# Performance work log

Measured on AMD Instinct MI355X. Metric: run time of the kernel, lower is better.

Reference implementation:

```python
import jax, jax.numpy as jnp
import numpy as np

TI, N, TO, D, H, FF, V, L = 128, 8, 32, 512, 8, 2048, 2000, 6


def _ln(x, s, b, eps=1e-5):
    m = jnp.mean(x, -1, keepdims=True)
    v = jnp.var(x, -1, keepdims=True)
    return (x - m) / jnp.sqrt(v + eps) * s + b


def _pos_enc(t, d):
    pos = np.arange(t)[:, None]
    div = np.exp(np.arange(0, d, 2) * (-np.log(10000.0) / d))
    pe = np.zeros((t, d), np.float32)
    pe[:, 0::2] = np.sin(pos * div)
    pe[:, 1::2] = np.cos(pos * div)
    return jnp.asarray(pe)


def _forward(enc_out, embed, enc_w, enc_b, qkv_w, qkv_b, o_w, o_b, ln1_s, ln1_b,
             ff1_w, ff1_b, ff2_w, ff2_b, ln2_s, ln2_b, out_w, tgt_pad, tgt_len, sos):
    n, to = tgt_pad.shape
    t = to + 1
    v, d = embed.shape
    hd = d // H
    # prepend <sos>, embed (scaled) + sinusoidal positions; dropout omitted (eval)
    tgt = jnp.pad(tgt_pad, ((0, 0), (1, 0)), constant_values=sos)  # N x T
    x = embed[tgt] * jnp.sqrt(jnp.float32(d)) + _pos_enc(t, d)[None]  # N x T x D
    x = x.transpose(1, 0, 2)  # T x N x D (time-major, pytorch default)
    causal = jnp.triu(jnp.ones((t, t), bool), k=1)  # True = masked
    lens = jnp.maximum(tgt_len, 1)
    pad = jnp.arange(t)[None, :] >= lens[:, None]  # N x T key padding
    mask = causal[None, None] | pad[:, None, None, :]
    neg = jnp.float32(-1e9)

    def heads(z):  # T x N x D -> N x H x T x hd
        return z.reshape(t, n, H, hd).transpose(1, 2, 0, 3)

    for l in range(L):  # post-norm TransformerEncoderLayer, relu FFN
        qkv = jnp.einsum('tnd,ed->tne', x, qkv_w[l]) + qkv_b[l]
        q, k_, v_ = jnp.split(qkv, 3, axis=-1)
        q = heads(q) / jnp.sqrt(jnp.float32(hd))
        k_, v_ = heads(k_), heads(v_)
        sc = jnp.einsum('nhqd,nhkd->nhqk', q, k_)
        att = jax.nn.softmax(jnp.where(mask, neg, sc), axis=-1)
        o = jnp.einsum('nhqk,nhkd->nhqd', att, v_).transpose(2, 0, 1, 3).reshape(t, n, d)
        o = jnp.einsum('tnd,ed->tne', o, o_w[l]) + o_b[l]
        x = _ln(x + o, ln1_s[l], ln1_b[l])
        h = jax.nn.relu(jnp.einsum('tnd,fd->tnf', x, ff1_w[l]) + ff1_b[l])
        h = jnp.einsum('tnf,df->tnd', h, ff2_w[l]) + ff2_b[l]
        x = _ln(x + h, ln2_s[l], ln2_b[l])

    enc = jnp.einsum('ind,ed->ine', enc_out, enc_w) + enc_b  # Ti x N x D
    add = jnp.tanh(enc[None] + x[:, None])  # (To+1) x Ti x N x D joiner
    out = jnp.einsum('tind,vd->tinv', add, out_w)  # (To+1) x Ti x N x V
    return out.transpose(2, 1, 0, 3)  # N x Ti x (To+1) x V


def setup_inputs() -> dict:
    key = jax.random.key(0)
    ks = jax.random.split(key, 12)
    s = 0.02
    return dict(
        enc_out=jax.random.normal(ks[0], (TI, N, D), jnp.float32),
        embed=jax.random.normal(ks[1], (V, D), jnp.float32) * s,
        enc_w=jax.random.normal(ks[2], (D, D), jnp.float32) * s,
        enc_b=jnp.zeros((D,), jnp.float32),
        qkv_w=jax.random.normal(ks[3], (L, 3 * D, D), jnp.float32) * s,
        qkv_b=jnp.zeros((L, 3 * D), jnp.float32),
        o_w=jax.random.normal(ks[4], (L, D, D), jnp.float32) * s,
        o_b=jnp.zeros((L, D), jnp.float32),
        ln1_s=jnp.ones((L, D), jnp.float32),
        ln1_b=jnp.zeros((L, D), jnp.float32),
        ff1_w=jax.random.normal(ks[5], (L, FF, D), jnp.float32) * s,
        ff1_b=jnp.zeros((L, FF), jnp.float32),
        ff2_w=jax.random.normal(ks[6], (L, D, FF), jnp.float32) * s,
        ff2_b=jnp.zeros((L, D), jnp.float32),
        ln2_s=jnp.ones((L, D), jnp.float32),
        ln2_b=jnp.zeros((L, D), jnp.float32),
        out_w=jax.random.normal(ks[7], (V, D), jnp.float32) * s,
        tgt_pad=jax.random.randint(ks[8], (N, TO), 0, V),
        tgt_len=jax.random.randint(ks[9], (N,), TO // 2, TO + 2),
        sos=1,
    )


def reference(enc_out, embed, enc_w, enc_b, qkv_w, qkv_b, o_w, o_b, ln1_s, ln1_b,
              ff1_w, ff1_b, ff2_w, ff2_b, ln2_s, ln2_b, out_w, tgt_pad, tgt_len, sos):
    return _forward(enc_out, embed, enc_w, enc_b, qkv_w, qkv_b, o_w, o_b, ln1_s, ln1_b,
                    ff1_w, ff1_b, ff2_w, ff2_b, ln2_s, ln2_b, out_w, tgt_pad, tgt_len, sos)
```

## Files before the change

### kernel.cpp

```cpp
#include <hip/hip_runtime.h>
#include <hip/hip_bf16.h>
#include <math.h>

#define TI 128
#define NB 8
#define TO 32
#define TT 33
#define D 512
#define NH 8
#define HD 64
#define FF 2048
#define V 2000
#define NL 6
#define NTOK (TT*NB)
#define MJ (NB*TI*TT)

typedef __attribute__((ext_vector_type(4))) float  f4;
typedef __attribute__((ext_vector_type(8))) short  shortx8;
typedef unsigned short u16;

__device__ __forceinline__ u16 f2bf(float f) {
    unsigned u = __float_as_uint(f);
    unsigned r = (u + 0x7fffu + ((u >> 16) & 1u)) >> 16;
    return (u16)r;
}
__device__ __forceinline__ float bf2f(u16 h) {
    return __uint_as_float(((unsigned)h) << 16);
}
__device__ __forceinline__ float wsum(float v) {
#pragma unroll
    for (int off = 32; off; off >>= 1) v += __shfl_xor(v, off, 64);
    return v;
}
__device__ __forceinline__ float wmax(float v) {
#pragma unroll
    for (int off = 32; off; off >>= 1) v = fmaxf(v, __shfl_xor(v, off, 64));
    return v;
}
__device__ __forceinline__ f4 mfma16(shortx8 a, shortx8 b, f4 c) {
    return __builtin_amdgcn_mfma_f32_16x16x32_bf16(a, b, c, 0, 0, 0);
}
__device__ __forceinline__ void async16(const void* g, void* l) {
    __builtin_amdgcn_global_load_lds(
        (const __attribute__((address_space(1))) unsigned int*)g,
        (__attribute__((address_space(3))) unsigned int*)l, 16, 0, 0);
}

__global__ __launch_bounds__(256) void convert_w(
    const float* __restrict__ q, const float* __restrict__ o,
    const float* __restrict__ f1, const float* __restrict__ f2,
    const float* __restrict__ e, u16* __restrict__ Wh, u16* __restrict__ Wl)
{
    int i4 = blockIdx.x * 256 + threadIdx.x;
    const float* src; int loc;
    if (i4 < 1179648)      { src = q;  loc = i4; }
    else if (i4 < 1572864) { src = o;  loc = i4 - 1179648; }
    else if (i4 < 3145728) { src = f1; loc = i4 - 1572864; }
    else if (i4 < 4718592) { src = f2; loc = i4 - 3145728; }
    else                   { src = e;  loc = i4 - 4718592; }
    f4 v = *(const f4*)(src + (size_t)loc * 4);
    ushort4 h, l;
    h.x = f2bf(v[0]); l.x = f2bf(v[0] - bf2f(h.x));
    h.y = f2bf(v[1]); l.y = f2bf(v[1] - bf2f(h.y));
    h.z = f2bf(v[2]); l.z = f2bf(v[2] - bf2f(h.z));
    h.w = f2bf(v[3]); l.w = f2bf(v[3] - bf2f(h.w));
    *(ushort4*)(Wh + (size_t)i4 * 4) = h;
    *(ushort4*)(Wl + (size_t)i4 * 4) = l;
}

__global__ __launch_bounds__(256) void convert_plane(
    const float* __restrict__ src, u16* __restrict__ dh, u16* __restrict__ dl, int n4)
{
    int i = blockIdx.x * 256 + threadIdx.x;
    if (i >= n4) return;
    f4 v = *(const f4*)(src + (size_t)i * 4);
    ushort4 h, l;
    h.x = f2bf(v[0]); l.x = f2bf(v[0] - bf2f(h.x));
    h.y = f2bf(v[1]); l.y = f2bf(v[1] - bf2f(h.y));
    h.z = f2bf(v[2]); l.z = f2bf(v[2] - bf2f(h.z));
    h.w = f2bf(v[3]); l.w = f2bf(v[3] - bf2f(h.w));
    *(ushort4*)(dh + (size_t)i * 4) = h;
    *(ushort4*)(dl + (size_t)i * 4) = l;
}

__global__ __launch_bounds__(256) void embed_kernel(
    const float* __restrict__ emb, const int* __restrict__ tgt_pad,
    const int* __restrict__ sos, float* __restrict__ x,
    u16* __restrict__ xh, u16* __restrict__ xl)
{
    int idx = blockIdx.x * 256 + threadIdx.x;
    if (idx >= NTOK * D) return;
    int d = idx & (D - 1);
    int row = idx >> 9;
    int t = row >> 3, n = row & 7;
    int tok = (t == 0) ? *sos : tgt_pad[n * TO + t - 1];
    float freq = __expf((float)(d & ~1) * (-0.017988946039015984f));
    float ang = (float)t * freq;
    float pe = (d & 1) ? cosf(ang) : sinf(ang);
    float v = emb[tok * D + d] * 22.627416997969522f + pe;
    x[idx] = v;
    u16 h = f2bf(v);
    xh[idx] = h;
    xl[idx] = f2bf(v - bf2f(h));
}

template<int MODE>
__global__ __launch_bounds__(256) void gemm_bf(
    const u16* __restrict__ Ah, const u16* __restrict__ Al, int lda,
    const u16* __restrict__ Bh, const u16* __restrict__ Bl, int ldb,
    const float* __restrict__ bias,
    float* __restrict__ C, u16* __restrict__ Ch, u16* __restrict__ Cl,
    int M, int N, int ldc, int ksteps)
{
    __shared__ u16 ls[4][64 * 64];
    const int tid = threadIdx.x, lane = tid & 63, w = tid >> 6;
    const int wr = (w >> 1) * 32, wc = (w & 1) * 32;
    const int m0 = blockIdx.x * 64, n0 = blockIdx.y * 64;
    const int qd = lane >> 4, mm = lane & 15;
    const int kb = (MODE == 1) ? (int)blockIdx.z * ksteps * 64 : 0;
    f4 acc[2][2] = {};
    const u16* Ab  = Ah + (size_t)m0 * lda + kb;
    const u16* Alb = Al + (size_t)m0 * lda + kb;
    const u16* Bb  = Bh + (size_t)n0 * ldb + kb;
    const u16* Blb = Bl + (size_t)n0 * ldb + kb;

    for (int it = 0; it < ksteps; ++it) {
        int k0 = it * 64;
        __syncthreads();
#pragma unroll
        for (int i = 0; i < 2; ++i) {
            int idx = tid + i * 256;
            int row = idx >> 3, c8 = (idx & 7) * 8;
            async16(Ab  + (size_t)row * lda + k0 + c8, &ls[0][idx * 8]);
            async16(Alb + (size_t)row * lda + k0 + c8, &ls[1][idx * 8]);
            async16(Bb  + (size_t)row * ldb + k0 + c8, &ls[2][idx * 8]);
            async16(Blb + (size_t)row * ldb + k0 + c8, &ls[3][idx * 8]);
        }
        __syncthreads();
#pragma unroll
        for (int kk = 0; kk < 2; ++kk) {
            shortx8 aH[2], aL[2], bH[2], bL[2];
#pragma unroll
            for (int rt = 0; rt < 2; ++rt) {
                int row = wr + rt * 16 + mm;
                aH[rt] = *(const shortx8*)&ls[0][row * 64 + kk * 32 + qd * 8];
                aL[rt] = *(const shortx8*)&ls[1][row * 64 + kk * 32 + qd * 8];
                int col = wc + rt * 16 + mm;
                bH[rt] = *(const shortx8*)&ls[2][col * 64 + kk * 32 + qd * 8];
                bL[rt] = *(const shortx8*)&ls[3][col * 64 + kk * 32 + qd * 8];
            }
#pragma unroll
            for (int rt = 0; rt < 2; ++rt)
#pragma unroll
                for (int ct = 0; ct < 2; ++ct) {
                    acc[rt][ct] = mfma16(aH[rt], bH[ct], acc[rt][ct]);
                    acc[rt][ct] = mfma16(aH[rt], bL[ct], acc[rt][ct]);
                    acc[rt][ct] = mfma16(aL[rt], bH[ct], acc[rt][ct]);
                }
        }
    }
    float* Cz = C;
    if (MODE == 1) Cz = C + (size_t)blockIdx.z * (size_t)M * ldc;
#pragma unroll
    for (int rt = 0; rt < 2; ++rt)
#pragma unroll
        for (int ct = 0; ct < 2; ++ct)
#pragma unroll
            for (int reg = 0; reg < 4; ++reg) {
                int grow = m0 + wr + rt * 16 + qd * 4 + reg;
                int gcol = n0 + wc + ct * 16 + mm;
                if (grow < M) {
                    float v = acc[rt][ct][reg];
                    if (MODE != 1) v += bias[gcol];
                    if (MODE == 2) {
                        v = fmaxf(v, 0.f);
                        u16 h = f2bf(v);
                        Ch[(size_t)grow * ldc + gcol] = h;
                        Cl[(size_t)grow * ldc + gcol] = f2bf(v - bf2f(h));
                    } else {
                        Cz[(size_t)grow * ldc + gcol] = v;
                    }
                }
            }
}

__global__ __launch_bounds__(256) void attn_kernel(
    const float* __restrict__ qkv, const int* __restrict__ tgt_len,
    u16* __restrict__ oh, u16* __restrict__ ol)
{
    const int n = blockIdx.x >> 3, h = blockIdx.x & 7;
    const int tid = threadIdx.x, lane = tid & 63, w = tid >> 6;
    __shared__ float sq[TT * HD];
    __shared__ float skT[HD * TT];
    __shared__ float sv[TT * HD];
    for (int idx = tid; idx < TT * HD; idx += 256) {
        int t = idx >> 6, d = idx & 63;
        size_t base = (size_t)(t * NB + n) * (3 * D) + h * HD + d;
        sq[idx] = qkv[base] * 0.125f;
        skT[d * TT + t] = qkv[base + D];
        sv[idx] = qkv[base + 2 * D];
    }
    int len = max(tgt_len[n], 1);
    __syncthreads();
    for (int r = w; r < TT; r += 4) {
        bool ok = (lane < TT) && (lane <= r) && (lane < len);
        float s = -INFINITY;
        if (ok) {
            float dot = 0.f;
#pragma unroll 8
            for (int d = 0; d < HD; ++d) dot += sq[r * HD + d] * skT[d * TT + lane];
            s = dot;
        }
        float mx = wmax(s);
        float e = ok ? __expf(s - mx) : 0.f;
        float sum = wsum(e);
        float att = e / sum;
        float o = 0.f;
#pragma unroll
        for (int k = 0; k < TT; ++k) {
            float a = __shfl(att, k, 64);
            o += a * sv[k * HD + lane];
        }
        size_t oi = (size_t)(r * NB + n) * D + h * HD + lane;
        u16 hh = f2bf(o);
        oh[oi] = hh;
        ol[oi] = f2bf(o - bf2f(hh));
    }
}

template<int NP, int BIAS>
__global__ __launch_bounds__(256) void add_ln(
    float* __restrict__ x, const float* __restrict__ r,
    const float* __restrict__ bias2,
    const float* __restrict__ s, const float* __restrict__ b,
    u16* __restrict__ xh, u16* __restrict__ xl)
{
    int row = blockIdx.x * 4 + (threadIdx.x >> 6);
    int lane = threadIdx.x & 63;
    if (row >= NTOK) return;
    float* xr = x + (size_t)row * D;
    f4 v1 = *(const f4*)(xr + lane * 4);
    f4 v2 = *(const f4*)(xr + 256 + lane * 4);
#pragma unroll
    for (int p = 0; p < NP; ++p) {
        const float* rr = r + (size_t)p * (NTOK * D) + (size_t)row * D;
        v1 += *(const f4*)(rr + lane * 4);
        v2 += *(const f4*)(rr + 256 + lane * 4);
    }
    if (BIAS) {
        v1 += *(const f4*)(bias2 + lane * 4);
        v2 += *(const f4*)(bias2 + 256 + lane * 4);
    }
    float sum = 0.f, sq = 0.f;
#pragma unroll
    for (int j = 0; j < 4; ++j) {
        sum += v1[j] + v2[j];
        sq += v1[j] * v1[j] + v2[j] * v2[j];
    }
    sum = wsum(sum); sq = wsum(sq);
    float mean = sum * (1.f / D);
    float var = sq * (1.f / D) - mean * mean;
    float rstd = rsqrtf(var + 1e-5f);
    f4 o1, o2;
    ushort4 h1, l1, h2, l2;
    u16 th, tl;
#pragma unroll
    for (int j = 0; j < 4; ++j) {
        int c1 = lane * 4 + j, c2 = c1 + 256;
        o1[j] = (v1[j] - mean) * rstd * s[c1] + b[c1];
        o2[j] = (v2[j] - mean) * rstd * s[c2] + b[c2];
    }
    th = f2bf(o1[0]); tl = f2bf(o1[0] - bf2f(th)); h1.x = th; l1.x = tl;
    th = f2bf(o1[1]); tl = f2bf(o1[1] - bf2f(th)); h1.y = th; l1.y = tl;
    th = f2bf(o1[2]); tl = f2bf(o1[2] - bf2f(th)); h1.z = th; l1.z = tl;
    th = f2bf(o1[3]); tl = f2bf(o1[3] - bf2f(th)); h1.w = th; l1.w = tl;
    th = f2bf(o2[0]); tl = f2bf(o2[0] - bf2f(th)); h2.x = th; l2.x = tl;
    th = f2bf(o2[1]); tl = f2bf(o2[1] - bf2f(th)); h2.y = th; l2.y = tl;
    th = f2bf(o2[2]); tl = f2bf(o2[2] - bf2f(th)); h2.z = th; l2.z = tl;
    th = f2bf(o2[3]); tl = f2bf(o2[3] - bf2f(th)); h2.w = th; l2.w = tl;
    *(f4*)(xr + lane * 4) = o1;
    *(f4*)(xr + 256 + lane * 4) = o2;
    *(ushort4*)(xh + (size_t)row * D + lane * 4) = h1;
    *(ushort4*)(xl + (size_t)row * D + lane * 4) = l1;
    *(ushort4*)(xh + (size_t)row * D + 256 + lane * 4) = h2;
    *(ushort4*)(xl + (size_t)row * D + 256 + lane * 4) = l2;
}

__global__ __launch_bounds__(256) void prep_joiner_A(
    const float* __restrict__ encb, const float* __restrict__ x,
    u16* __restrict__ Aj)
{
    int idx = blockIdx.x * 256 + threadIdx.x;
    int d8 = (idx & 63) << 3;
    int row = idx >> 6;
    int n = row / (TI * TT);
    int rem = row - n * (TI * TT);
    int ti = rem / TT;
    int t = rem - ti * TT;
    const float* pe = encb + (size_t)(ti * NB + n) * D + d8;
    const float* px = x + (size_t)(t * NB + n) * D + d8;
    f4 e0 = *(const f4*)pe, e1 = *(const f4*)(pe + 4);
    f4 x0 = *(const f4*)px, x1 = *(const f4*)(px + 4);
    u16* dst = Aj + (size_t)row * D + d8;
#pragma unroll
    for (int j = 0; j < 4; ++j) {
        dst[j] = f2bf(tanhf(e0[j] + x0[j]));
        dst[4 + j] = f2bf(tanhf(e1[j] + x1[j]));
    }
}

__global__ __launch_bounds__(256) void prep_joiner_B(
    const float* __restrict__ out_w, u16* __restrict__ Bj)
{
    int idx = blockIdx.x * 256 + threadIdx.x;
    int d8 = (idx & 63) << 3;
    int row = idx >> 6;
    u16* dst = Bj + (size_t)row * D + d8;
    if (row < V) {
        const float* p = out_w + (size_t)row * D + d8;
        f4 a = *(const f4*)p, b = *(const f4*)(p + 4);
#pragma unroll
        for (int j = 0; j < 4; ++j) { dst[j] = f2bf(a[j]); dst[4 + j] = f2bf(b[j]); }
    } else {
#pragma unroll
        for (int j = 0; j < 8; ++j) dst[j] = 0;
    }
}

__global__ __launch_bounds__(256) void joiner_gemm(
    const u16* __restrict__ Aj, const u16* __restrict__ Bj,
    float* __restrict__ out)
{
    __shared__ u16 lsA[128 * 32];
    __shared__ u16 lsB[128 * 32];
    const int bid = blockIdx.x;
    const int mt = bid >> 4, nt = bid & 15;
    const int tid = threadIdx.x, lane = tid & 63, w = tid >> 6;
    const int wr = (w >> 1) * 64, wc = (w & 1) * 64;
    const int qd = lane >> 4, mm = lane & 15;
    f4 acc[4][4] = {};
    const u16* Abase = Aj + (size_t)mt * 128 * D;
    const u16* Bbase = Bj + (size_t)nt * 128 * D;

    for (int k0 = 0; k0 < D; k0 += 32) {
        __syncthreads();
#pragma unroll
        for (int i = 0; i < 2; ++i) {
            int idx = tid + i * 256;
            int row = idx >> 2, c = idx & 3;
            int chunk = c ^ ((row >> 1) & 3);
            async16(Abase + (size_t)row * D + k0 + chunk * 8, lsA + idx * 8);
            async16(Bbase + (size_t)row * D + k0 + chunk * 8, lsB + idx * 8);
        }
        __syncthreads();
        shortx8 af[4], bf[4];
#pragma unroll
        for (int rt = 0; rt < 4; ++rt) {
            int row = wr + rt * 16 + mm;
            int cpos = qd ^ ((row >> 1) & 3);
            af[rt] = *(const shortx8*)(lsA + row * 32 + cpos * 8);
        }
#pragma unroll
        for (int ct = 0; ct < 4; ++ct) {
            int col = wc + ct * 16 + mm;
            int cpos = qd ^ ((col >> 1) & 3);
            bf[ct] = *(const shortx8*)(lsB + col * 32 + cpos * 8);
        }
#pragma unroll
        for (int rt = 0; rt < 4; ++rt)
#pragma unroll
            for (int ct = 0; ct < 4; ++ct)
                acc[rt][ct] = mfma16(af[rt], bf[ct], acc[rt][ct]);
    }
#pragma unroll
    for (int rt = 0; rt < 4; ++rt)
#pragma unroll
        for (int ct = 0; ct < 4; ++ct)
#pragma unroll
            for (int reg = 0; reg < 4; ++reg) {
                int grow = mt * 128 + wr + rt * 16 + qd * 4 + reg;
                int gcol = nt * 128 + wc + ct * 16 + mm;
                if (gcol < V) out[(size_t)grow * V + gcol] = acc[rt][ct][reg];
            }
}

extern "C" void kernel_launch(void* const* d_in, const int* in_sizes, int n_in,
                              void* d_out, int out_size, void* d_ws, size_t ws_size,
                              hipStream_t stream)
{
    const float* enc_out = (const float*)d_in[0];
    const float* embed_w = (const float*)d_in[1];
    const float* enc_w   = (const float*)d_in[2];
    const float* enc_b   = (const float*)d_in[3];
    const float* qkv_w   = (const float*)d_in[4];
    const float* qkv_b   = (const float*)d_in[5];
    const float* o_w     = (const float*)d_in[6];
    const float* o_b     = (const float*)d_in[7];
    const float* ln1_s   = (const float*)d_in[8];
    const float* ln1_b   = (const float*)d_in[9];
    const float* ff1_w   = (const float*)d_in[10];
    const float* ff1_b   = (const float*)d_in[11];
    const float* ff2_w   = (const float*)d_in[12];
    const float* ff2_b   = (const float*)d_in[13];
    const float* ln2_s   = (const float*)d_in[14];
    const float* ln2_b   = (const float*)d_in[15];
    const float* out_w   = (const float*)d_in[16];
    const int*   tgt_pad = (const int*)d_in[17];
    const int*   tgt_len = (const int*)d_in[18];
    const int*   sos     = (const int*)d_in[19];

    float* ws = (float*)d_ws;
    float* x    = ws;
    float* qkvb = ws + 135168;
    float* tmp  = ws + 540672;
    float* part = ws + 675840;
    float* encb = ws + 1216512;
    u16* u  = (u16*)(ws + 1740800);
    u16* xh = u;                  u16* xl = xh + 320 * 512;
    u16* oh = xl + 163840;        u16* ol = oh + 163840;
    u16* hh = ol + 163840;        u16* hl = hh + 320 * 2048;
    u16* eh = hl + 655360;        u16* el = eh + 524288;
    u16* Wh = el + 524288;        u16* Wl = Wh + 19136512;
    u16* Aj = Wl + 19136512;      u16* Bj = Aj + (size_t)MJ * D;

    const size_t QO = 0;
    const size_t OO = 4718592;
    const size_t F1 = 6291456;
    const size_t F2 = 12582912;
    const size_t EW = 18874368;

    convert_w<<<18688, 256, 0, stream>>>(qkv_w, o_w, ff1_w, ff2_w, enc_w, Wh, Wl);
    convert_plane<<<512, 256, 0, stream>>>(enc_out, eh, el, 131072);
    embed_kernel<<<528, 256, 0, stream>>>(embed_w, tgt_pad, sos, x, xh, xl);
    for (int l = 0; l < NL; ++l) {
        gemm_bf<0><<<dim3(5, 24), 256, 0, stream>>>(
            xh, xl, 512, Wh + QO + (size_t)l * 786432, Wl + QO + (size_t)l * 786432, 512,
            qkv_b + l * 1536, qkvb, nullptr, nullptr, NTOK, 1536, 1536, 8);
        attn_kernel<<<NB * NH, 256, 0, stream>>>(qkvb, tgt_len, oh, ol);
        gemm_bf<0><<<dim3(5, 8), 256, 0, stream>>>(
            oh, ol, 512, Wh + OO + (size_t)l * 262144, Wl + OO + (size_t)l * 262144, 512,
            o_b + l * 512, tmp, nullptr, nullptr, NTOK, 512, 512, 8);
        add_ln<1, 0><<<66, 256, 0, stream>>>(
            x, tmp, nullptr, ln1_s + l * 512, ln1_b + l * 512, xh, xl);
        gemm_bf<2><<<dim3(5, 32), 256, 0, stream>>>(
            xh, xl, 512, Wh + F1 + (size_t)l * 1048576, Wl + F1 + (size_t)l * 1048576, 512,
            ff1_b + l * 2048, nullptr, hh, hl, NTOK, 2048, 2048, 8);
        gemm_bf<1><<<dim3(5, 8, 4), 256, 0, stream>>>(
            hh, hl, 2048, Wh + F2 + (size_t)l * 1048576, Wl + F2 + (size_t)l * 1048576, 2048,
            nullptr, part, nullptr, nullptr, NTOK, 512, 512, 8);
        add_ln<4, 1><<<66, 256, 0, stream>>>(
            x, part, ff2_b + l * 512, ln2_s + l * 512, ln2_b + l * 512, xh, xl);
    }
    gemm_bf<0><<<dim3(16, 8), 256, 0, stream>>>(
        eh, el, 512, Wh + EW, Wl + EW, 512,
        enc_b, encb, nullptr, nullptr, TI * NB, 512, 512, 8);
    prep_joiner_A<<<(MJ * D / 8) / 256, 256, 0, stream>>>(encb, x, Aj);
    prep_joiner_B<<<(2048 * D / 8) / 256, 256, 0, stream>>>(out_w, Bj);
    joiner_gemm<<<264 * 16, 256, 0, stream>>>(Aj, Bj, (float*)d_out);
}
```

Baseline: 975.7 us.

## Fuse decoder layers into one persistent kernel with software grid barriers

Replaces the roughly 36 per-layer kernel launches with a single persistent kernel of 256 blocks. An atomic-counter grid barrier separates the stages, and the encoder projection GEMM runs alongside the first QKV GEMM. The output projection now uses split-K writing into partial buffers, with its bias folded into the add+LN step. The convert/embed kernels and the two joiner prep kernels are each merged into one launch. This cuts launch gaps and tail effects, at the cost of spin-wait barriers and idle blocks in small stages, and it relies on all 256 blocks being co-resident.

```diff
diff --git a/kernel.cpp b/kernel.cpp
--- a/kernel.cpp
+++ b/kernel.cpp
@@ -14,10 +14,17 @@
 #define NL 6
 #define NTOK (TT*NB)
 #define MJ (NB*TI*TT)
+#define GRID 256
 
 typedef __attribute__((ext_vector_type(4))) float  f4;
 typedef __attribute__((ext_vector_type(8))) short  shortx8;
 typedef unsigned short u16;
+
+static constexpr size_t QO = 0;
+static constexpr size_t OO = 4718592;
+static constexpr size_t F1 = 6291456;
+static constexpr size_t F2 = 12582912;
+static constexpr size_t EW = 18874368;
 
 __device__ __forceinline__ u16 f2bf(float f) {
     unsigned u = __float_as_uint(f);
@@ -46,78 +53,92 @@
         (__attribute__((address_space(3))) unsigned int*)l, 16, 0, 0);
 }
 
-__global__ __launch_bounds__(256) void convert_w(
-    const float* __restrict__ q, const float* __restrict__ o,
-    const float* __restrict__ f1, const float* __restrict__ f2,
-    const float* __restrict__ e, u16* __restrict__ Wh, u16* __restrict__ Wl)
-{
-    int i4 = blockIdx.x * 256 + threadIdx.x;
-    const float* src; int loc;
-    if (i4 < 1179648)      { src = q;  loc = i4; }
-    else if (i4 < 1572864) { src = o;  loc = i4 - 1179648; }
-    else if (i4 < 3145728) { src = f1; loc = i4 - 1572864; }
-    else if (i4 < 4718592) { src = f2; loc = i4 - 3145728; }
-    else                   { src = e;  loc = i4 - 4718592; }
-    f4 v = *(const f4*)(src + (size_t)loc * 4);
-    ushort4 h, l;
-    h.x = f2bf(v[0]); l.x = f2bf(v[0] - bf2f(h.x));
-    h.y = f2bf(v[1]); l.y = f2bf(v[1] - bf2f(h.y));
-    h.z = f2bf(v[2]); l.z = f2bf(v[2] - bf2f(h.z));
-    h.w = f2bf(v[3]); l.w = f2bf(v[3] - bf2f(h.w));
-    *(ushort4*)(Wh + (size_t)i4 * 4) = h;
-    *(ushort4*)(Wl + (size_t)i4 * 4) = l;
-}
-
-__global__ __launch_bounds__(256) void convert_plane(
-    const float* __restrict__ src, u16* __restrict__ dh, u16* __restrict__ dl, int n4)
-{
-    int i = blockIdx.x * 256 + threadIdx.x;
-    if (i >= n4) return;
-    f4 v = *(const f4*)(src + (size_t)i * 4);
-    ushort4 h, l;
-    h.x = f2bf(v[0]); l.x = f2bf(v[0] - bf2f(h.x));
-    h.y = f2bf(v[1]); l.y = f2bf(v[1] - bf2f(h.y));
-    h.z = f2bf(v[2]); l.z = f2bf(v[2] - bf2f(h.z));
-    h.w = f2bf(v[3]); l.w = f2bf(v[3] - bf2f(h.w));
-    *(ushort4*)(dh + (size_t)i * 4) = h;
-    *(ushort4*)(dl + (size_t)i * 4) = l;
-}
-
-__global__ __launch_bounds__(256) void embed_kernel(
+__device__ __forceinline__ void grid_sync(unsigned* bar) {
+    __syncthreads();
+    if (threadIdx.x == 0) {
+        __threadfence();
+        unsigned my = __hip_atomic_fetch_add(bar, 1u, __ATOMIC_RELAXED,
+                                             __HIP_MEMORY_SCOPE_AGENT);
+        unsigned target = (my / (unsigned)GRID + 1u) * (unsigned)GRID;
+        while (__hip_atomic_load(bar, __ATOMIC_RELAXED,
+                                 __HIP_MEMORY_SCOPE_AGENT) < target)
+            __builtin_amdgcn_s_sleep(4);
+        __threadfence();
+    }
+    __syncthreads();
+}
+
+__global__ __launch_bounds__(256) void fused_convert(
+    const float* __restrict__ qw, const float* __restrict__ ow,
+    const float* __restrict__ f1w, const float* __restrict__ f2w,
+    const float* __restrict__ ew, u16* __restrict__ Wh, u16* __restrict__ Wl,
+    const float* __restrict__ enc_out, u16* __restrict__ eh, u16* __restrict__ el,
     const float* __restrict__ emb, const int* __restrict__ tgt_pad,
     const int* __restrict__ sos, float* __restrict__ x,
-    u16* __restrict__ xh, u16* __restrict__ xl)
-{
-    int idx = blockIdx.x * 256 + threadIdx.x;
-    if (idx >= NTOK * D) return;
-    int d = idx & (D - 1);
-    int row = idx >> 9;
-    int t = row >> 3, n = row & 7;
-    int tok = (t == 0) ? *sos : tgt_pad[n * TO + t - 1];
-    float freq = __expf((float)(d & ~1) * (-0.017988946039015984f));
-    float ang = (float)t * freq;
-    float pe = (d & 1) ? cosf(ang) : sinf(ang);
-    float v = emb[tok * D + d] * 22.627416997969522f + pe;
-    x[idx] = v;
-    u16 h = f2bf(v);
-    xh[idx] = h;
-    xl[idx] = f2bf(v - bf2f(h));
+    u16* __restrict__ xh, u16* __restrict__ xl, unsigned* __restrict__ bar)
+{
+    const int bid = blockIdx.x, tid = threadIdx.x;
+    if (bid == 0 && tid == 0)
+        __hip_atomic_store(bar, 0u, __ATOMIC_RELEASE, __HIP_MEMORY_SCOPE_AGENT);
+    if (bid < 18688) {
+        int i4 = bid * 256 + tid;
+        const float* src; int loc;
+        if (i4 < 1179648)      { src = qw;  loc = i4; }
+        else if (i4 < 1572864) { src = ow;  loc = i4 - 1179648; }
+        else if (i4 < 3145728) { src = f1w; loc = i4 - 1572864; }
+        else if (i4 < 4718592) { src = f2w; loc = i4 - 3145728; }
+        else                   { src = ew;  loc = i4 - 4718592; }
+        f4 v = *(const f4*)(src + (size_t)loc * 4);
+        ushort4 h, l;
+        h.x = f2bf(v[0]); l.x = f2bf(v[0] - bf2f(h.x));
+        h.y = f2bf(v[1]); l.y = f2bf(v[1] - bf2f(h.y));
+        h.z = f2bf(v[2]); l.z = f2bf(v[2] - bf2f(h.z));
+        h.w = f2bf(v[3]); l.w = f2bf(v[3] - bf2f(h.w));
+        *(ushort4*)(Wh + (size_t)i4 * 4) = h;
+        *(ushort4*)(Wl + (size_t)i4 * 4) = l;
+    } else if (bid < 19200) {
+        int i = (bid - 18688) * 256 + tid;
+        f4 v = *(const f4*)(enc_out + (size_t)i * 4);
+        ushort4 h, l;
+        h.x = f2bf(v[0]); l.x = f2bf(v[0] - bf2f(h.x));
+        h.y = f2bf(v[1]); l.y = f2bf(v[1] - bf2f(h.y));
+        h.z = f2bf(v[2]); l.z = f2bf(v[2] - bf2f(h.z));
+        h.w = f2bf(v[3]); l.w = f2bf(v[3] - bf2f(h.w));
+        *(ushort4*)(eh + (size_t)i * 4) = h;
+        *(ushort4*)(el + (size_t)i * 4) = l;
+    } else {
+        int idx = (bid - 19200) * 256 + tid;
+        if (idx < NTOK * D) {
+            int d = idx & (D - 1);
+            int row = idx >> 9;
+            int t = row >> 3, n = row & 7;
+            int tok = (t == 0) ? *sos : tgt_pad[n * TO + t - 1];
+            float freq = __expf((float)(d & ~1) * (-0.017988946039015984f));
+            float ang = (float)t * freq;
+            float pe = (d & 1) ? cosf(ang) : sinf(ang);
+            float v = emb[tok * D + d] * 22.627416997969522f + pe;
+            x[idx] = v;
+            u16 h = f2bf(v);
+            xh[idx] = h;
+            xl[idx] = f2bf(v - bf2f(h));
+        }
+    }
 }
 
 template<int MODE>
-__global__ __launch_bounds__(256) void gemm_bf(
+__device__ void gemm_tile(
+    u16 (*ls)[64 * 64], int mt, int nt, int zz,
     const u16* __restrict__ Ah, const u16* __restrict__ Al, int lda,
     const u16* __restrict__ Bh, const u16* __restrict__ Bl, int ldb,
     const float* __restrict__ bias,
     float* __restrict__ C, u16* __restrict__ Ch, u16* __restrict__ Cl,
-    int M, int N, int ldc, int ksteps)
-{
-    __shared__ u16 ls[4][64 * 64];
+    int M, int ldc, int ksteps)
+{
     const int tid = threadIdx.x, lane = tid & 63, w = tid >> 6;
     const int wr = (w >> 1) * 32, wc = (w & 1) * 32;
-    const int m0 = blockIdx.x * 64, n0 = blockIdx.y * 64;
+    const int m0 = mt * 64, n0 = nt * 64;
     const int qd = lane >> 4, mm = lane & 15;
-    const int kb = (MODE == 1) ? (int)blockIdx.z * ksteps * 64 : 0;
+    const int kb = (MODE == 1) ? zz * ksteps * 64 : 0;
     f4 acc[2][2] = {};
     const u16* Ab  = Ah + (size_t)m0 * lda + kb;
     const u16* Alb = Al + (size_t)m0 * lda + kb;
@@ -160,7 +181,7 @@
         }
     }
     float* Cz = C;
-    if (MODE == 1) Cz = C + (size_t)blockIdx.z * (size_t)M * ldc;
+    if (MODE == 1) Cz = C + (size_t)zz * (size_t)M * ldc;
 #pragma unroll
     for (int rt = 0; rt < 2; ++rt)
 #pragma unroll
@@ -184,15 +205,16 @@
             }
 }
 
-__global__ __launch_bounds__(256) void attn_kernel(
-    const float* __restrict__ qkv, const int* __restrict__ tgt_len,
-    u16* __restrict__ oh, u16* __restrict__ ol)
-{
-    const int n = blockIdx.x >> 3, h = blockIdx.x & 7;
+__device__ void attn_body(u16* lsr, int bid,
+                          const float* __restrict__ qkv,
+                          const int* __restrict__ tgt_len,
+                          u16* __restrict__ oh, u16* __restrict__ ol)
+{
+    const int n = bid >> 3, h = bid & 7;
     const int tid = threadIdx.x, lane = tid & 63, w = tid >> 6;
-    __shared__ float sq[TT * HD];
-    __shared__ float skT[HD * TT];
-    __shared__ float sv[TT * HD];
+    float* sq  = (float*)lsr;
+    float* skT = sq + TT * HD;
+    float* sv  = skT + HD * TT;
     for (int idx = tid; idx < TT * HD; idx += 256) {
         int t = idx >> 6, d = idx & 63;
         size_t base = (size_t)(t * NB + n) * (3 * D) + h * HD + d;
@@ -222,20 +244,20 @@
             o += a * sv[k * HD + lane];
         }
         size_t oi = (size_t)(r * NB + n) * D + h * HD + lane;
-        u16 hh = f2bf(o);
-        oh[oi] = hh;
-        ol[oi] = f2bf(o - bf2f(hh));
+        u16 hv = f2bf(o);
+        oh[oi] = hv;
+        ol[oi] = f2bf(o - bf2f(hv));
     }
 }
 
 template<int NP, int BIAS>
-__global__ __launch_bounds__(256) void add_ln(
+__device__ void add_ln_body(int bid,
     float* __restrict__ x, const float* __restrict__ r,
     const float* __restrict__ bias2,
     const float* __restrict__ s, const float* __restrict__ b,
     u16* __restrict__ xh, u16* __restrict__ xl)
 {
-    int row = blockIdx.x * 4 + (threadIdx.x >> 6);
+    int row = bid * 4 + (threadIdx.x >> 6);
     int lane = threadIdx.x & 63;
     if (row >= NTOK) return;
     float* xr = x + (size_t)row * D;
@@ -286,44 +308,124 @@
     *(ushort4*)(xl + (size_t)row * D + 256 + lane * 4) = l2;
 }
 
-__global__ __launch_bounds__(256) void prep_joiner_A(
+__global__ __launch_bounds__(256, 1) void decoder_coop(
+    const u16* __restrict__ Wh, const u16* __restrict__ Wl,
+    const float* __restrict__ qkv_b, const float* __restrict__ o_b,
+    const float* __restrict__ ln1_s, const float* __restrict__ ln1_b,
+    const float* __restrict__ ff1_b, const float* __restrict__ ff2_b,
+    const float* __restrict__ ln2_s, const float* __restrict__ ln2_b,
+    const float* __restrict__ enc_b, const int* __restrict__ tgt_len,
+    float* __restrict__ x, float* __restrict__ qkvb,
+    float* __restrict__ part, float* __restrict__ encb,
+    u16* __restrict__ xh, u16* __restrict__ xl,
+    u16* __restrict__ oh, u16* __restrict__ ol,
+    u16* __restrict__ hh, u16* __restrict__ hl,
+    const u16* __restrict__ eh, const u16* __restrict__ el,
+    unsigned* __restrict__ bar)
+{
+    __shared__ u16 ls[4][64 * 64];
+    const int bid = blockIdx.x;
+
+    for (int l = 0; l < NL; ++l) {
+        const u16* WqH = Wh + QO + (size_t)l * 786432;
+        const u16* WqL = Wl + QO + (size_t)l * 786432;
+        const u16* WoH = Wh + OO + (size_t)l * 262144;
+        const u16* WoL = Wl + OO + (size_t)l * 262144;
+        const u16* W1H = Wh + F1 + (size_t)l * 1048576;
+        const u16* W1L = Wl + F1 + (size_t)l * 1048576;
+        const u16* W2H = Wh + F2 + (size_t)l * 1048576;
+        const u16* W2L = Wl + F2 + (size_t)l * 1048576;
+
+        if (bid < 120) {
+            gemm_tile<0>(ls, bid / 24, bid % 24, 0,
+                         xh, xl, 512, WqH, WqL, 512,
+                         qkv_b + l * 1536, qkvb, nullptr, nullptr,
+                         NTOK, 1536, 8);
+        } else if (l == 0 && bid < 248) {
+            int t = bid - 120;
+            gemm_tile<0>(ls, t >> 3, t & 7, 0,
+                         eh, el, 512, Wh + EW, Wl + EW, 512,
+                         enc_b, encb, nullptr, nullptr,
+                         TI * NB, 512, 8);
+        }
+        grid_sync(bar);
+
+        if (bid < NB * NH) attn_body((u16*)ls, bid, qkvb, tgt_len, oh, ol);
+        grid_sync(bar);
+
+        if (bid < 160) {
+            int z = bid / 40, r = bid - z * 40;
+            gemm_tile<1>(ls, r / 8, r % 8, z,
+                         oh, ol, 512, WoH, WoL, 512,
+                         nullptr, part, nullptr, nullptr,
+                         NTOK, 512, 2);
+        }
+        grid_sync(bar);
+
+        if (bid < 66) add_ln_body<4, 1>(bid, x, part, o_b + l * 512,
+                                        ln1_s + l * 512, ln1_b + l * 512, xh, xl);
+        grid_sync(bar);
+
+        if (bid < 160) {
+            gemm_tile<2>(ls, bid / 32, bid % 32, 0,
+                         xh, xl, 512, W1H, W1L, 512,
+                         ff1_b + l * 2048, nullptr, hh, hl,
+                         NTOK, 2048, 8);
+        }
+        grid_sync(bar);
+
+        if (bid < 160) {
+            int z = bid / 40, r = bid - z * 40;
+            gemm_tile<1>(ls, r / 8, r % 8, z,
+                         hh, hl, 2048, W2H, W2L, 2048,
+                         nullptr, part, nullptr, nullptr,
+                         NTOK, 512, 8);
+        }
+        grid_sync(bar);
+
+        if (bid < 66) add_ln_body<4, 1>(bid, x, part, ff2_b + l * 512,
+                                        ln2_s + l * 512, ln2_b + l * 512, xh, xl);
+        if (l < NL - 1) grid_sync(bar);
+    }
+}
+
+__global__ __launch_bounds__(256) void prep_joiner(
     const float* __restrict__ encb, const float* __restrict__ x,
-    u16* __restrict__ Aj)
-{
-    int idx = blockIdx.x * 256 + threadIdx.x;
-    int d8 = (idx & 63) << 3;
-    int row = idx >> 6;
-    int n = row / (TI * TT);
-    int rem = row - n * (TI * TT);
-    int ti = rem / TT;
-    int t = rem - ti * TT;
-    const float* pe = encb + (size_t)(ti * NB + n) * D + d8;
-    const float* px = x + (size_t)(t * NB + n) * D + d8;
-    f4 e0 = *(const f4*)pe, e1 = *(const f4*)(pe + 4);
-    f4 x0 = *(const f4*)px, x1 = *(const f4*)(px + 4);
-    u16* dst = Aj + (size_t)row * D + d8;
-#pragma unroll
-    for (int j = 0; j < 4; ++j) {
-        dst[j] = f2bf(tanhf(e0[j] + x0[j]));
-        dst[4 + j] = f2bf(tanhf(e1[j] + x1[j]));
-    }
-}
-
-__global__ __launch_bounds__(256) void prep_joiner_B(
-    const float* __restrict__ out_w, u16* __restrict__ Bj)
-{
-    int idx = blockIdx.x * 256 + threadIdx.x;
-    int d8 = (idx & 63) << 3;
-    int row = idx >> 6;
-    u16* dst = Bj + (size_t)row * D + d8;
-    if (row < V) {
-        const float* p = out_w + (size_t)row * D + d8;
-        f4 a = *(const f4*)p, b = *(const f4*)(p + 4);
-#pragma unroll
-        for (int j = 0; j < 4; ++j) { dst[j] = f2bf(a[j]); dst[4 + j] = f2bf(b[j]); }
+    u16* __restrict__ Aj, const float* __restrict__ out_w, u16* __restrict__ Bj)
+{
+    const int bid = blockIdx.x;
+    if (bid < 8448) {
+        int idx = bid * 256 + threadIdx.x;
+        int d8 = (idx & 63) << 3;
+        int row = idx >> 6;
+        int n = row / (TI * TT);
+        int rem = row - n * (TI * TT);
+        int ti = rem / TT;
+        int t = rem - ti * TT;
+        const float* pe = encb + (size_t)(ti * NB + n) * D + d8;
+        const float* px = x + (size_t)(t * NB + n) * D + d8;
+        f4 e0 = *(const f4*)pe, e1 = *(const f4*)(pe + 4);
+        f4 x0 = *(const f4*)px, x1 = *(const f4*)(px + 4);
+        u16* dst = Aj + (size_t)row * D + d8;
+#pragma unroll
+        for (int j = 0; j < 4; ++j) {
+            dst[j] = f2bf(tanhf(e0[j] + x0[j]));
+            dst[4 + j] = f2bf(tanhf(e1[j] + x1[j]));
+        }
     } else {
-#pragma unroll
-        for (int j = 0; j < 8; ++j) dst[j] = 0;
+        int idx = (bid - 8448) * 256 + threadIdx.x;
+        int d8 = (idx & 63) << 3;
+        int row = idx >> 6;
+        u16* dst = Bj + (size_t)row * D + d8;
+        if (row < V) {
+            const float* p = out_w + (size_t)row * D + d8;
+            f4 a = *(const f4*)p, b = *(const f4*)(p + 4);
+#pragma unroll
+            for (int j = 0; j < 4; ++j) { dst[j] = f2bf(a[j]); dst[4 + j] = f2bf(b[j]); }
+        } else {
+#pragma unroll
+            for (int j = 0; j < 8; ++j) dst[j] = 0;
+        }
     }
 }
 
@@ -412,7 +514,7 @@
     float* ws = (float*)d_ws;
     float* x    = ws;
     float* qkvb = ws + 135168;
-    float* tmp  = ws + 540672;
+    unsigned* bar = (unsigned*)(ws + 540672);
     float* part = ws + 675840;
     float* encb = ws + 1216512;
     u16* u  = (u16*)(ws + 1740800);
@@ -423,38 +525,16 @@
     u16* Wh = el + 524288;        u16* Wl = Wh + 19136512;
     u16* Aj = Wl + 19136512;      u16* Bj = Aj + (size_t)MJ * D;
 
-    const size_t QO = 0;
-    const size_t OO = 4718592;
-    const size_t F1 = 6291456;
-    const size_t F2 = 12582912;
-    const size_t EW = 18874368;
-
-    convert_w<<<18688, 256, 0, stream>>>(qkv_w, o_w, ff1_w, ff2_w, enc_w, Wh, Wl);
-    convert_plane<<<512, 256, 0, stream>>>(enc_out, eh, el, 131072);
-    embed_kernel<<<528, 256, 0, stream>>>(embed_w, tgt_pad, sos, x, xh, xl);
-    for (int l = 0; l < NL; ++l) {
-        gemm_bf<0><<<dim3(5, 24), 256, 0, stream>>>(
-            xh, xl, 512, Wh + QO + (size_t)l * 786432, Wl + QO + (size_t)l * 786432, 512,
-            qkv_b + l * 1536, qkvb, nullptr, nullptr, NTOK, 1536, 1536, 8);
-        attn_kernel<<<NB * NH, 256, 0, stream>>>(qkvb, tgt_len, oh, ol);
-        gemm_bf<0><<<dim3(5, 8), 256, 0, stream>>>(
-            oh, ol, 512, Wh + OO + (size_t)l * 262144, Wl + OO + (size_t)l * 262144, 512,
-            o_b + l * 512, tmp, nullptr, nullptr, NTOK, 512, 512, 8);
-        add_ln<1, 0><<<66, 256, 0, stream>>>(
-            x, tmp, nullptr, ln1_s + l * 512, ln1_b + l * 512, xh, xl);
-        gemm_bf<2><<<dim3(5, 32), 256, 0, stream>>>(
-            xh, xl, 512, Wh + F1 + (size_t)l * 1048576, Wl + F1 + (size_t)l * 1048576, 512,
-            ff1_b + l * 2048, nullptr, hh, hl, NTOK, 2048, 2048, 8);
-        gemm_bf<1><<<dim3(5, 8, 4), 256, 0, stream>>>(
-            hh, hl, 2048, Wh + F2 + (size_t)l * 1048576, Wl + F2 + (size_t)l * 1048576, 2048,
-            nullptr, part, nullptr, nullptr, NTOK, 512, 512, 8);
-        add_ln<4, 1><<<66, 256, 0, stream>>>(
-            x, part, ff2_b + l * 512, ln2_s + l * 512, ln2_b + l * 512, xh, xl);
-    }
-    gemm_bf<0><<<dim3(16, 8), 256, 0, stream>>>(
-        eh, el, 512, Wh + EW, Wl + EW, 512,
-        enc_b, encb, nullptr, nullptr, TI * NB, 512, 512, 8);
-    prep_joiner_A<<<(MJ * D / 8) / 256, 256, 0, stream>>>(encb, x, Aj);
-    prep_joiner_B<<<(2048 * D / 8) / 256, 256, 0, stream>>>(out_w, Bj);
+    fused_convert<<<19728, 256, 0, stream>>>(
+        qkv_w, o_w, ff1_w, ff2_w, enc_w, Wh, Wl,
+        enc_out, eh, el, embed_w, tgt_pad, sos, x, xh, xl, bar);
+
+    decoder_coop<<<GRID, 256, 0, stream>>>(
+        Wh, Wl, qkv_b, o_b, ln1_s, ln1_b, ff1_b, ff2_b, ln2_s, ln2_b,
+        enc_b, tgt_len, x, qkvb, part, encb,
+        xh, xl, oh, ol, hh, hl, eh, el, bar);
+
+    prep_joiner<<<8960, 256, 0, stream>>>(encb, x, Aj, out_w, Bj);
+
     joiner_gemm<<<264 * 16, 256, 0, stream>>>(Aj, Bj, (float*)d_out);
 }
```

New measurement: 1.684 ms. 1.73x slower.
